# Kernel tuning notes

Measured on AMD Instinct MI355X. Metric: run time of the kernel, lower is better.

Reference implementation:

```python
import jax, jax.numpy as jnp
import numpy as np

B, S, D, H = 4, 2048, 768, 4
DH = D // H  # 192


def setup_inputs() -> dict:
    key = jax.random.key(0)
    ks = jax.random.split(key, 5)
    std = 1.0 / np.sqrt(D)
    return {
        "x": jax.random.normal(ks[0], (B, S, D), dtype=jnp.float32),
        "Wq": jax.random.normal(ks[1], (D, D), dtype=jnp.float32) * std,
        "Wk": jax.random.normal(ks[2], (D, D), dtype=jnp.float32) * std,
        "Wv": jax.random.normal(ks[3], (D, D), dtype=jnp.float32) * std,
        "Wo": jax.random.normal(ks[4], (D, D), dtype=jnp.float32) * std,
    }


def reference(x, Wq, Wk, Wv, Wo):
    b, s, d = x.shape
    # nn.Linear(bias=False): y = x @ W.T
    q = (x @ Wq.T).reshape(b, s, H, DH).transpose(0, 2, 1, 3)  # [B,H,S,DH]
    k = (x @ Wk.T).reshape(b, s, H, DH).transpose(0, 2, 1, 3)
    v = (x @ Wv.T).reshape(b, s, H, DH).transpose(0, 2, 1, 3)
    scale = jnp.sqrt(jnp.asarray(DH, dtype=q.dtype))
    logits = jnp.einsum("bhqd,bhkd->bhqk", q, k) / scale  # [B,H,S,S]
    causal = jnp.tril(jnp.ones((s, s), dtype=bool))
    logits = jnp.where(causal, logits, -jnp.inf)
    A = jax.nn.softmax(logits, axis=-1)
    preout = jnp.einsum("bhqk,bhkd->bhqd", A, v)  # [B,H,S,DH]
    # W_O = rearrange(Wo.T, '(h dh) dm -> h dh dm'); sum over heads == full Wo
    W_O = Wo.T.reshape(H, DH, D)
    out = jnp.einsum("bhsd,hdm->bsm", preout, W_O)  # [B,S,D]
    return out
```

## Files before the change

kernel.cpp:

```cpp
#include <hip/hip_runtime.h>
#include <hip/hip_bf16.h>

constexpr int CB = 4, CS = 2048, CD = 768, CH = 4, CDH = 192;
constexpr int CM = CB * CS;

typedef float f32x4 __attribute__((ext_vector_type(4)));
typedef float fx4 __attribute__((ext_vector_type(4)));
typedef __bf16 bx8 __attribute__((ext_vector_type(8)));
typedef unsigned short u16;
typedef u16 u16x8 __attribute__((ext_vector_type(8)));
typedef u16 u16x4 __attribute__((ext_vector_type(4)));

static __device__ __forceinline__ u16 f32_bf16(float f) {
  unsigned u = __builtin_bit_cast(unsigned, f);
  u += 0x7FFFu + ((u >> 16) & 1u);
  return (u16)(u >> 16);
}
static __device__ __forceinline__ float bf16_f32(u16 v) {
  return __builtin_bit_cast(float, (unsigned)v << 16);
}

static __device__ __forceinline__ f32x4 mfma16(bx8 a, bx8 b, f32x4 c) {
  return __builtin_amdgcn_mfma_f32_16x16x32_bf16(a, b, c, 0, 0, 0);
}

__global__ void __launch_bounds__(256) convert_all(
    const float* __restrict__ x, const float* __restrict__ wq,
    const float* __restrict__ wk, const float* __restrict__ wv,
    const float* __restrict__ wo, u16* __restrict__ xb, u16* __restrict__ wqb,
    u16* __restrict__ wkb, u16* __restrict__ wvb, u16* __restrict__ wob) {
  const float* srcs[5] = {x, wq, wk, wv, wo};
  u16* dsts[5] = {xb, wqb, wkb, wvb, wob};
  const int n4s[5] = {CM * CD / 4, CD * CD / 4, CD * CD / 4, CD * CD / 4,
                      CD * CD / 4};
  const int gsz = gridDim.x * blockDim.x;
  const int gid = blockIdx.x * blockDim.x + threadIdx.x;
#pragma unroll
  for (int sg = 0; sg < 5; ++sg) {
    const fx4* src = (const fx4*)srcs[sg];
    u16* dst = dsts[sg];
    const int n4 = n4s[sg];
    for (int i = gid; i < n4; i += gsz) {
      fx4 v = src[i];
      u16x4 o;
      o[0] = f32_bf16(v[0]);
      o[1] = f32_bf16(v[1]);
      o[2] = f32_bf16(v[2]);
      o[3] = f32_bf16(v[3]);
      *(u16x4*)&dst[(size_t)i * 4] = o;
    }
  }
}

template <bool OUT_BF16>
__global__ void __launch_bounds__(256) gemm_bt(
    const u16* __restrict__ A, const u16* __restrict__ Bw0,
    const u16* __restrict__ Bw1, const u16* __restrict__ Bw2,
    void* __restrict__ C0, void* __restrict__ C1, void* __restrict__ C2,
    int M, int N, int K) {
  constexpr int LDK = 72;
  __shared__ u16 As[128][LDK];
  __shared__ u16 Bs[128][LDK];
  const int z = blockIdx.z;
  const u16* Bw = (z == 0) ? Bw0 : ((z == 1) ? Bw1 : Bw2);
  void* Cv = (z == 0) ? C0 : ((z == 1) ? C1 : C2);
  const int m0 = blockIdx.x * 128;
  const int n0 = blockIdx.y * 128;
  const int tid = threadIdx.x;
  const int wave = tid >> 6, lane = tid & 63;
  const int wr = wave >> 1, wc = wave & 1;
  const int lr = lane & 15, lhi = lane >> 4;

  f32x4 acc[4][4];
  const f32x4 zero = {0.f, 0.f, 0.f, 0.f};
#pragma unroll
  for (int i = 0; i < 4; ++i)
#pragma unroll
    for (int j = 0; j < 4; ++j) acc[i][j] = zero;

  u16x8 areg[4], breg[4];
  auto ldregs = [&](int kk) {
#pragma unroll
    for (int r = 0; r < 4; ++r) {
      const int id = tid + r * 256;
      const int row = id >> 3, ch = id & 7;
      areg[r] = *(const u16x8*)&A[(size_t)(m0 + row) * K + kk + ch * 8];
      breg[r] = *(const u16x8*)&Bw[(size_t)(n0 + row) * K + kk + ch * 8];
    }
  };

  ldregs(0);
  for (int kk = 0; kk < K; kk += 64) {
    __syncthreads();
#pragma unroll
    for (int r = 0; r < 4; ++r) {
      const int id = tid + r * 256;
      const int row = id >> 3, ch = id & 7;
      *(u16x8*)&As[row][ch * 8] = areg[r];
      *(u16x8*)&Bs[row][ch * 8] = breg[r];
    }
    if (kk + 64 < K) ldregs(kk + 64);
    __syncthreads();
#pragma unroll
    for (int ks = 0; ks < 2; ++ks) {
      bx8 af[4], bf[4];
#pragma unroll
      for (int mf = 0; mf < 4; ++mf)
        af[mf] = *(const bx8*)&As[wr * 64 + mf * 16 + lr][ks * 32 + lhi * 8];
#pragma unroll
      for (int nf = 0; nf < 4; ++nf)
        bf[nf] = *(const bx8*)&Bs[wc * 64 + nf * 16 + lr][ks * 32 + lhi * 8];
      __builtin_amdgcn_s_setprio(1);
#pragma unroll
      for (int mf = 0; mf < 4; ++mf)
#pragma unroll
        for (int nf = 0; nf < 4; ++nf)
          acc[mf][nf] = mfma16(af[mf], bf[nf], acc[mf][nf]);
      __builtin_amdgcn_s_setprio(0);
    }
  }
#pragma unroll
  for (int mf = 0; mf < 4; ++mf)
#pragma unroll
    for (int nf = 0; nf < 4; ++nf)
#pragma unroll
      for (int r = 0; r < 4; ++r) {
        const int row = m0 + wr * 64 + mf * 16 + lhi * 4 + r;
        const int col = n0 + wc * 64 + nf * 16 + lr;
        if constexpr (OUT_BF16)
          ((u16*)Cv)[(size_t)row * N + col] = f32_bf16(acc[mf][nf][r]);
        else
          ((float*)Cv)[(size_t)row * N + col] = acc[mf][nf][r];
      }
}

__global__ void __launch_bounds__(256, 2) flash_attn(
    const u16* __restrict__ Qg, const u16* __restrict__ Kg,
    const u16* __restrict__ Vg, u16* __restrict__ Og, u16* __restrict__ paO,
    float* __restrict__ paML, u16* __restrict__ pbO,
    float* __restrict__ pbML) {
  __shared__ u16 Ks[12288];
  __shared__ u16 Vs[12288];
  __shared__ u16 Ps[4][16][72];
  const int i0_ = blockIdx.x;
  const int xcd = i0_ & 7;
  const int j_ = i0_ >> 3;
  const int bh = xcd * 2 + (j_ >> 5);
  const int jj = j_ & 31;
  const int t = jj >> 1;
  const int roleB = jj & 1;
  const int qtLo = t, qtHi = 31 - t;
  const int slot = bh * 16 + (15 - t);
  const int b = bh >> 2, h = bh & 3;
  const int tid = threadIdx.x;
  const int wave = tid >> 6, lane = tid & 63;
  const int lr = lane & 15, lhi = lane >> 4;
  const size_t base_elem = ((size_t)b * CS) * CD + (size_t)h * CDH;
  constexpr float scale = 0.07216878364870323f;
  const f32x4 zero = {0.f, 0.f, 0.f, 0.f};

  int kOff[6], vOff[6];
#pragma unroll
  for (int r = 0; r < 6; ++r) {
    const int p = tid + r * 256;
    {
      const int k = p / 24, c16 = p - k * 24;
      const unsigned swz = ((unsigned)(c16 * 16)) ^ ((unsigned)((k & 7) << 4));
      kOff[r] = k * CD + (int)(swz >> 1);
    }
    {
      const int blk = p >> 3, kq = (p >> 1) & 3, dh = p & 1;
      const int kk = ((blk & 15) << 2) + kq;
      const int d = ((blk >> 4) << 4) + dh * 8;
      vOff[r] = kk * CD + d;
    }
  }
  const unsigned vlds0 =
      (unsigned)(unsigned long long)(__attribute__((address_space(3)))
                                         u16*)&Vs[0];

  float m_run, l_run;
  f32x4 acc[12];
  bx8 qf[6];
  u16x8 kreg[6], vreg[6];

  auto qload = [&](int qt) {
    const size_t qoff = base_elem + (size_t)(qt * 64 + wave * 16 + lr) * CD;
#pragma unroll
    for (int c = 0; c < 6; ++c)
      qf[c] = *(const bx8*)&Qg[qoff + c * 32 + lhi * 8];
  };

  auto ldregs = [&](int kt) {
    const u16* kg = Kg + base_elem + (size_t)(kt * 64) * CD;
    const u16* vg = Vg + base_elem + (size_t)(kt * 64) * CD;
#pragma unroll
    for (int r = 0; r < 6; ++r) {
      kreg[r] = *(const u16x8*)&kg[kOff[r]];
      vreg[r] = *(const u16x8*)&vg[vOff[r]];
    }
  };

  auto compute = [&](int i, int qt) {
    const int qg = qt * 64 + wave * 16 + lr;
    const int k0 = i * 64;
    const bool diag = (i == qt);
    f32x4 st[4];
#pragma unroll
    for (int mf = 0; mf < 4; ++mf) st[mf] = zero;
    __builtin_amdgcn_s_setprio(1);
#pragma unroll
    for (int c = 0; c < 6; ++c)
#pragma unroll
      for (int mf = 0; mf < 4; ++mf) {
        const int row = mf * 16 + lr;
        const unsigned off =
            ((unsigned)(c * 64 + lhi * 16)) ^ ((unsigned)((row & 7) << 4));
        const bx8 kf =
            *(const bx8*)((const char*)Ks + (size_t)row * 384 + off);
        st[mf] = mfma16(kf, qf[c], st[mf]);
      }
    __builtin_amdgcn_s_setprio(0);
    float pvv[16];
#pragma unroll
    for (int mf = 0; mf < 4; ++mf)
#pragma unroll
      for (int r = 0; r < 4; ++r) {
        float s = st[mf][r] * scale;
        if (diag && (k0 + mf * 16 + lhi * 4 + r > qg)) s = -INFINITY;
        pvv[mf * 4 + r] = s;
      }
    float mx = pvv[0];
#pragma unroll
    for (int tt = 1; tt < 16; ++tt) mx = fmaxf(mx, pvv[tt]);
    mx = fmaxf(mx, __shfl_xor(mx, 16, 64));
    mx = fmaxf(mx, __shfl_xor(mx, 32, 64));
    const bool skip = __all(mx - m_run <= 8.0f);
    if (!skip) {
      const float mnew = fmaxf(m_run, mx);
      const float alpha = __expf(m_run - mnew);
      float afr[4];
#pragma unroll
      for (int r = 0; r < 4; ++r) afr[r] = __shfl(alpha, lhi * 4 + r, 64);
#pragma unroll
      for (int nf = 0; nf < 12; ++nf)
#pragma unroll
        for (int r = 0; r < 4; ++r) acc[nf][r] *= afr[r];
      l_run *= alpha;
      m_run = mnew;
    }
    float rs = 0.f;
#pragma unroll
    for (int tt = 0; tt < 16; ++tt) {
      const float e = __expf(pvv[tt] - m_run);
      pvv[tt] = e;
      rs += e;
    }
    rs += __shfl_xor(rs, 16, 64);
    rs += __shfl_xor(rs, 32, 64);
    l_run += rs;
#pragma unroll
    for (int mf = 0; mf < 4; ++mf)
#pragma unroll
      for (int rp = 0; rp < 2; ++rp) {
        const unsigned w0 = f32_bf16(pvv[mf * 4 + rp * 2]);
        const unsigned w1 = f32_bf16(pvv[mf * 4 + rp * 2 + 1]);
        *(unsigned*)&Ps[wave][lr][mf * 16 + lhi * 4 + rp * 2] =
            w0 | (w1 << 16);
      }
    const bx8 pf0 = *(const bx8*)&Ps[wave][lr][lhi * 8];
    const bx8 pf1 = *(const bx8*)&Ps[wave][lr][32 + lhi * 8];
#pragma unroll
    for (int gg = 0; gg < 3; ++gg) {
      u16x4 tl[4][2], th[4][2];
#pragma unroll
      for (int q4 = 0; q4 < 4; ++q4)
#pragma unroll
        for (int c2 = 0; c2 < 2; ++c2) {
          const int nf = gg * 4 + q4;
          const unsigned va =
              vlds0 + (unsigned)((nf * 16 + c2 * 8 + lhi * 2) * 128 + lr * 8);
          asm volatile("ds_read_b64_tr_b16 %0, %2\n\t"
                       "ds_read_b64_tr_b16 %1, %2 offset:128"
                       : "=&v"(tl[q4][c2]), "=&v"(th[q4][c2])
                       : "v"(va));
        }
      asm volatile("s_waitcnt lgkmcnt(0)" ::: "memory");
      __builtin_amdgcn_sched_barrier(0);
      __builtin_amdgcn_s_setprio(1);
#pragma unroll
      for (int q4 = 0; q4 < 4; ++q4)
#pragma unroll
        for (int c2 = 0; c2 < 2; ++c2) {
          const int nf = gg * 4 + q4;
          const u16x8 vv = __builtin_shufflevector(tl[q4][c2], th[q4][c2], 0,
                                                   1, 2, 3, 4, 5, 6, 7);
          acc[nf] = mfma16(c2 == 0 ? pf0 : pf1, __builtin_bit_cast(bx8, vv),
                           acc[nf]);
        }
      __builtin_amdgcn_s_setprio(0);
    }
  };

  auto run = [&](int qt, int i0, int i1) {
    m_run = -INFINITY;
    l_run = 0.f;
#pragma unroll
    for (int nf = 0; nf < 12; ++nf) acc[nf] = zero;
    qload(qt);
    ldregs(i0);
    for (int i = i0; i <= i1; ++i) {
      __syncthreads();
#pragma unroll
      for (int r = 0; r < 6; ++r) {
        *(u16x8*)&Ks[(size_t)(tid + r * 256) * 8] = kreg[r];
        *(u16x8*)&Vs[(size_t)(tid + r * 256) * 8] = vreg[r];
      }
      if (i < i1) ldregs(i + 1);
      __syncthreads();
      compute(i, qt);
    }
  };

  auto final_epilogue = [&](int qt) {
#pragma unroll
    for (int r = 0; r < 4; ++r) {
      const float lb = __shfl(l_run, lhi * 4 + r, 64);
      const float linv = 1.0f / lb;
      const size_t orow =
          base_elem + (size_t)(qt * 64 + wave * 16 + lhi * 4 + r) * CD;
#pragma unroll
      for (int nf = 0; nf < 12; ++nf)
        Og[orow + nf * 16 + lr] = f32_bf16(acc[nf][r] * linv);
    }
  };

  auto partial_epilogue = [&](u16* pO, float* pML) {
    if (lhi == 0) {
      pML[slot * 128 + wave * 16 + lr] = m_run;
      pML[slot * 128 + 64 + wave * 16 + lr] = l_run;
    }
#pragma unroll
    for (int r = 0; r < 4; ++r) {
      const float lb = __shfl(l_run, lhi * 4 + r, 64);
      const float linv = 1.0f / lb;
      u16* dst =
          pO + (size_t)slot * 12288 + (size_t)(wave * 16 + lhi * 4 + r) * 192;
#pragma unroll
      for (int nf = 0; nf < 12; ++nf)
        dst[nf * 16 + lr] = f32_bf16(acc[nf][r] * linv);
    }
  };

  if (roleB) {
    run(qtHi, 15 - t, 31 - t);
    partial_epilogue(pbO, pbML);
  } else {
    run(qtLo, 0, t);
    final_epilogue(qtLo);
    if (t < 15) {
      run(qtHi, 0, 14 - t);
      partial_epilogue(paO, paML);
    } else {
      if (tid < 64) {
        paML[slot * 128 + tid] = -1e30f;
        paML[slot * 128 + 64 + tid] = 0.f;
      }
    }
  }
}

__global__ void __launch_bounds__(256) combine_qt(
    const u16* __restrict__ paO, const float* __restrict__ paML,
    const u16* __restrict__ pbO, const float* __restrict__ pbML,
    u16* __restrict__ Og) {
  const int s = blockIdx.x;
  const int bh = s >> 4;
  const int qtHi = 16 + (s & 15);
  const int b = bh >> 2, h = bh & 3;
  const int tid = threadIdx.x;
  const int row = tid >> 2, cg = tid & 3;
  const float mA = paML[s * 128 + row], lA = paML[s * 128 + 64 + row];
  const float mB = pbML[s * 128 + row], lB = pbML[s * 128 + 64 + row];
  const size_t obase =
      ((size_t)b * CS + (size_t)qtHi * 64 + row) * CD + h * CDH + cg * 48;
  const u16* pa = paO + (size_t)s * 12288 + (size_t)row * 192 + cg * 48;
  const u16* pb = pbO + (size_t)s * 12288 + (size_t)row * 192 + cg * 48;
  if (lA > 0.f) {
    const float M = fmaxf(mA, mB);
    const float wA = lA * __expf(mA - M), wB = lB * __expf(mB - M);
    const float inv = 1.0f / (wA + wB);
    const float fa = wA * inv, fb = wB * inv;
#pragma unroll
    for (int c = 0; c < 6; ++c) {
      const u16x8 va = *(const u16x8*)&pa[c * 8];
      const u16x8 vb = *(const u16x8*)&pb[c * 8];
      u16x8 o;
#pragma unroll
      for (int j = 0; j < 8; ++j)
        o[j] = f32_bf16(fa * bf16_f32(va[j]) + fb * bf16_f32(vb[j]));
      *(u16x8*)&Og[obase + c * 8] = o;
    }
  } else {
#pragma unroll
    for (int c = 0; c < 6; ++c)
      *(u16x8*)&Og[obase + c * 8] = *(const u16x8*)&pb[c * 8];
  }
}

extern "C" void kernel_launch(void* const* d_in, const int* in_sizes, int n_in,
                              void* d_out, int out_size, void* d_ws,
                              size_t ws_size, hipStream_t stream) {
  (void)in_sizes;
  (void)n_in;
  (void)out_size;
  (void)ws_size;
  const float* x = (const float*)d_in[0];
  const float* wq = (const float*)d_in[1];
  const float* wk = (const float*)d_in[2];
  const float* wv = (const float*)d_in[3];
  const float* wo = (const float*)d_in[4];
  float* out = (float*)d_out;
  char* ws = (char*)d_ws;
  const size_t big = (size_t)CM * CD * 2;
  const size_t wsz = (size_t)CD * CD * 2;
  u16* xb = (u16*)ws;
  u16* qb = (u16*)(ws + big);
  u16* kb = (u16*)(ws + 2 * big);
  u16* vb = (u16*)(ws + 3 * big);
  u16* wqb = (u16*)(ws + 4 * big);
  u16* wkb = (u16*)(ws + 4 * big + wsz);
  u16* wvb = (u16*)(ws + 4 * big + 2 * wsz);
  u16* wob = (u16*)(ws + 4 * big + 3 * wsz);
  u16* pob = xb;
  const size_t pOsz = (size_t)256 * 64 * 192 * 2;
  u16* paO = (u16*)d_out;
  u16* pbO = (u16*)((char*)d_out + pOsz);
  float* paML = (float*)((char*)d_out + 2 * pOsz);
  float* pbML = (float*)((char*)d_out + 2 * pOsz + 131072);

  convert_all<<<dim3(1024), dim3(256), 0, stream>>>(x, wq, wk, wv, wo, xb, wqb,
                                                    wkb, wvb, wob);
  gemm_bt<true><<<dim3(64, 6, 3), dim3(256), 0, stream>>>(
      xb, wqb, wkb, wvb, (void*)qb, (void*)kb, (void*)vb, CM, CD, CD);
  flash_attn<<<dim3(512), dim3(256), 0, stream>>>(qb, kb, vb, pob, paO, paML,
                                                  pbO, pbML);
  combine_qt<<<dim3(256), dim3(256), 0, stream>>>(paO, paML, pbO, pbML, pob);
  gemm_bt<false><<<dim3(64, 6, 1), dim3(256), 0, stream>>>(
      pob, wob, wob, wob, (void*)out, (void*)out, (void*)out, CM, CD, CD);
}
```

Measured before the change: 139.2 us.

## Double-buffer K in LDS and split QK/PV phases in flash attention

Adds a second LDS buffer for K so the next K tile is stored while the current one is used. K loads are issued two tiles ahead and V one tile ahead. The compute step is split so the QK^T and softmax phase runs before the barrier and P·V after it, overlapping global loads with compute. P scratch now uses an XOR-swizzled unpadded layout to avoid bank conflicts, and the convert kernel grid is doubled. This raises LDS use per block, which may hurt occupancy at 2 blocks per CU.

```diff
diff --git a/kernel.cpp b/kernel.cpp
--- a/kernel.cpp
+++ b/kernel.cpp
@@ -139,9 +139,9 @@
     const u16* __restrict__ Vg, u16* __restrict__ Og, u16* __restrict__ paO,
     float* __restrict__ paML, u16* __restrict__ pbO,
     float* __restrict__ pbML) {
-  __shared__ u16 Ks[12288];
+  __shared__ u16 Kbuf[2][12288];
   __shared__ u16 Vs[12288];
-  __shared__ u16 Ps[4][16][72];
+  __shared__ u16 Ps[4][16][64];
   const int i0_ = blockIdx.x;
   const int xcd = i0_ & 7;
   const int j_ = i0_ >> 3;
@@ -191,20 +191,22 @@
       qf[c] = *(const bx8*)&Qg[qoff + c * 32 + lhi * 8];
   };
 
-  auto ldregs = [&](int kt) {
+  auto kload = [&](int kt) {
     const u16* kg = Kg + base_elem + (size_t)(kt * 64) * CD;
+#pragma unroll
+    for (int r = 0; r < 6; ++r) kreg[r] = *(const u16x8*)&kg[kOff[r]];
+  };
+  auto vload = [&](int kt) {
     const u16* vg = Vg + base_elem + (size_t)(kt * 64) * CD;
 #pragma unroll
-    for (int r = 0; r < 6; ++r) {
-      kreg[r] = *(const u16x8*)&kg[kOff[r]];
-      vreg[r] = *(const u16x8*)&vg[vOff[r]];
-    }
-  };
-
-  auto compute = [&](int i, int qt) {
+    for (int r = 0; r < 6; ++r) vreg[r] = *(const u16x8*)&vg[vOff[r]];
+  };
+
+  auto compute_qkt_sm = [&](int i, int qt, int cur) {
     const int qg = qt * 64 + wave * 16 + lr;
     const int k0 = i * 64;
     const bool diag = (i == qt);
+    const char* ksb = (const char*)&Kbuf[cur][0];
     f32x4 st[4];
 #pragma unroll
     for (int mf = 0; mf < 4; ++mf) st[mf] = zero;
@@ -216,8 +218,7 @@
         const int row = mf * 16 + lr;
         const unsigned off =
             ((unsigned)(c * 64 + lhi * 16)) ^ ((unsigned)((row & 7) << 4));
-        const bx8 kf =
-            *(const bx8*)((const char*)Ks + (size_t)row * 384 + off);
+        const bx8 kf = *(const bx8*)(ksb + (size_t)row * 384 + off);
         st[mf] = mfma16(kf, qf[c], st[mf]);
       }
     __builtin_amdgcn_s_setprio(0);
@@ -265,11 +266,18 @@
       for (int rp = 0; rp < 2; ++rp) {
         const unsigned w0 = f32_bf16(pvv[mf * 4 + rp * 2]);
         const unsigned w1 = f32_bf16(pvv[mf * 4 + rp * 2 + 1]);
-        *(unsigned*)&Ps[wave][lr][mf * 16 + lhi * 4 + rp * 2] =
-            w0 | (w1 << 16);
-      }
-    const bx8 pf0 = *(const bx8*)&Ps[wave][lr][lhi * 8];
-    const bx8 pf1 = *(const bx8*)&Ps[wave][lr][32 + lhi * 8];
+        const unsigned pbyte =
+            (unsigned)(wave * 2048 + lr * 128 +
+                       ((mf * 32 + lhi * 8 + rp * 4) ^ ((lr & 7) << 4)));
+        *(unsigned*)((char*)Ps + pbyte) = w0 | (w1 << 16);
+      }
+  };
+
+  auto compute_pv = [&]() {
+    const bx8 pf0 = *(const bx8*)((const char*)Ps + wave * 2048 + lr * 128 +
+                                  ((lhi * 16) ^ ((lr & 7) << 4)));
+    const bx8 pf1 = *(const bx8*)((const char*)Ps + wave * 2048 + lr * 128 +
+                                  ((64 + lhi * 16) ^ ((lr & 7) << 4)));
 #pragma unroll
     for (int gg = 0; gg < 3; ++gg) {
       u16x4 tl[4][2], th[4][2];
@@ -308,17 +316,30 @@
 #pragma unroll
     for (int nf = 0; nf < 12; ++nf) acc[nf] = zero;
     qload(qt);
-    ldregs(i0);
+    kload(i0);
+    __syncthreads();
+#pragma unroll
+    for (int r = 0; r < 6; ++r)
+      *(u16x8*)&Kbuf[0][(size_t)(tid + r * 256) * 8] = kreg[r];
+    vload(i0);
+    if (i0 + 1 <= i1) kload(i0 + 1);
+    int cur = 0;
     for (int i = i0; i <= i1; ++i) {
       __syncthreads();
 #pragma unroll
-      for (int r = 0; r < 6; ++r) {
-        *(u16x8*)&Ks[(size_t)(tid + r * 256) * 8] = kreg[r];
+      for (int r = 0; r < 6; ++r)
         *(u16x8*)&Vs[(size_t)(tid + r * 256) * 8] = vreg[r];
-      }
-      if (i < i1) ldregs(i + 1);
+      if (i < i1) {
+#pragma unroll
+        for (int r = 0; r < 6; ++r)
+          *(u16x8*)&Kbuf[cur ^ 1][(size_t)(tid + r * 256) * 8] = kreg[r];
+        vload(i + 1);
+      }
+      if (i + 2 <= i1) kload(i + 2);
+      compute_qkt_sm(i, qt, cur);
       __syncthreads();
-      compute(i, qt);
+      compute_pv();
+      cur ^= 1;
     }
   };
 
@@ -439,7 +460,7 @@
   float* paML = (float*)((char*)d_out + 2 * pOsz);
   float* pbML = (float*)((char*)d_out + 2 * pOsz + 131072);
 
-  convert_all<<<dim3(1024), dim3(256), 0, stream>>>(x, wq, wk, wv, wo, xb, wqb,
+  convert_all<<<dim3(2048), dim3(256), 0, stream>>>(x, wq, wk, wv, wo, xb, wqb,
                                                     wkb, wvb, wob);
   gemm_bt<true><<<dim3(64, 6, 3), dim3(256), 0, stream>>>(
       xb, wqb, wkb, wvb, (void*)qb, (void*)kb, (void*)vb, CM, CD, CD);
```

New measurement: 156.4 us. +12.4%, slower.

## Double-buffer GEMM tiles with direct global-to-LDS loads and XOR swizzle

Applied to the files above, without the earlier changes.

The bf16 GEMM now stages A/B tiles straight from global memory into LDS using global_load_lds, instead of going through registers. It double-buffers the tiles so the next K-slice loads while MFMAs run on the current one. It also XOR-swizzles the LDS layout in place of row padding, to avoid bank conflicts. The convert kernel grid is doubled. LDS use rises to 64KB per block, which may lower occupancy, and the single barrier per iteration relies on the hardware waiting for the direct LDS loads to finish.

```diff
diff --git a/kernel.cpp b/kernel.cpp
--- a/kernel.cpp
+++ b/kernel.cpp
@@ -22,6 +22,12 @@
 
 static __device__ __forceinline__ f32x4 mfma16(bx8 a, bx8 b, f32x4 c) {
   return __builtin_amdgcn_mfma_f32_16x16x32_bf16(a, b, c, 0, 0, 0);
+}
+
+static __device__ __forceinline__ void load_lds16(const u16* g, u16* l) {
+  __builtin_amdgcn_global_load_lds(
+      (const __attribute__((address_space(1))) unsigned int*)g,
+      (__attribute__((address_space(3))) unsigned int*)l, 16, 0, 0);
 }
 
 __global__ void __launch_bounds__(256) convert_all(
@@ -58,9 +64,8 @@
     const u16* __restrict__ Bw1, const u16* __restrict__ Bw2,
     void* __restrict__ C0, void* __restrict__ C1, void* __restrict__ C2,
     int M, int N, int K) {
-  constexpr int LDK = 72;
-  __shared__ u16 As[128][LDK];
-  __shared__ u16 Bs[128][LDK];
+  __shared__ u16 As[2][8192];
+  __shared__ u16 Bs[2][8192];
   const int z = blockIdx.z;
   const u16* Bw = (z == 0) ? Bw0 : ((z == 1) ? Bw1 : Bw2);
   void* Cv = (z == 0) ? C0 : ((z == 1) ? C1 : C2);
@@ -78,38 +83,47 @@
 #pragma unroll
     for (int j = 0; j < 4; ++j) acc[i][j] = zero;
 
-  u16x8 areg[4], breg[4];
-  auto ldregs = [&](int kk) {
+  int sOff[4];
+#pragma unroll
+  for (int r = 0; r < 4; ++r) {
+    const int p = tid + r * 256;
+    const int row = p >> 3, ch = p & 7;
+    sOff[r] = row * K +
+              (int)(((unsigned)(ch * 16) ^ ((unsigned)((row & 7) << 4))) >> 1);
+  }
+  const u16* Ag = A + (size_t)m0 * K;
+  const u16* Bg = Bw + (size_t)n0 * K;
+
+  auto stage = [&](int buf, int kk) {
 #pragma unroll
     for (int r = 0; r < 4; ++r) {
-      const int id = tid + r * 256;
-      const int row = id >> 3, ch = id & 7;
-      areg[r] = *(const u16x8*)&A[(size_t)(m0 + row) * K + kk + ch * 8];
-      breg[r] = *(const u16x8*)&Bw[(size_t)(n0 + row) * K + kk + ch * 8];
-    }
-  };
-
-  ldregs(0);
+      load_lds16(Ag + kk + sOff[r], &As[buf][(size_t)(tid + r * 256) * 8]);
+      load_lds16(Bg + kk + sOff[r], &Bs[buf][(size_t)(tid + r * 256) * 8]);
+    }
+  };
+
+  stage(0, 0);
+  __syncthreads();
+  int buf = 0;
   for (int kk = 0; kk < K; kk += 64) {
-    __syncthreads();
-#pragma unroll
-    for (int r = 0; r < 4; ++r) {
-      const int id = tid + r * 256;
-      const int row = id >> 3, ch = id & 7;
-      *(u16x8*)&As[row][ch * 8] = areg[r];
-      *(u16x8*)&Bs[row][ch * 8] = breg[r];
-    }
-    if (kk + 64 < K) ldregs(kk + 64);
-    __syncthreads();
+    if (kk + 64 < K) stage(buf ^ 1, kk + 64);
 #pragma unroll
     for (int ks = 0; ks < 2; ++ks) {
       bx8 af[4], bf[4];
 #pragma unroll
-      for (int mf = 0; mf < 4; ++mf)
-        af[mf] = *(const bx8*)&As[wr * 64 + mf * 16 + lr][ks * 32 + lhi * 8];
-#pragma unroll
-      for (int nf = 0; nf < 4; ++nf)
-        bf[nf] = *(const bx8*)&Bs[wc * 64 + nf * 16 + lr][ks * 32 + lhi * 8];
+      for (int mf = 0; mf < 4; ++mf) {
+        const int row = wr * 64 + mf * 16 + lr;
+        const unsigned off =
+            ((unsigned)(ks * 64 + lhi * 16)) ^ ((unsigned)((row & 7) << 4));
+        af[mf] = *(const bx8*)((const char*)&As[buf][0] + row * 128 + off);
+      }
+#pragma unroll
+      for (int nf = 0; nf < 4; ++nf) {
+        const int row = wc * 64 + nf * 16 + lr;
+        const unsigned off =
+            ((unsigned)(ks * 64 + lhi * 16)) ^ ((unsigned)((row & 7) << 4));
+        bf[nf] = *(const bx8*)((const char*)&Bs[buf][0] + row * 128 + off);
+      }
       __builtin_amdgcn_s_setprio(1);
 #pragma unroll
       for (int mf = 0; mf < 4; ++mf)
@@ -118,6 +132,8 @@
           acc[mf][nf] = mfma16(af[mf], bf[nf], acc[mf][nf]);
       __builtin_amdgcn_s_setprio(0);
     }
+    __syncthreads();
+    buf ^= 1;
   }
 #pragma unroll
   for (int mf = 0; mf < 4; ++mf)
@@ -439,7 +455,7 @@
   float* paML = (float*)((char*)d_out + 2 * pOsz);
   float* pbML = (float*)((char*)d_out + 2 * pOsz + 131072);
 
-  convert_all<<<dim3(1024), dim3(256), 0, stream>>>(x, wq, wk, wv, wo, xb, wqb,
+  convert_all<<<dim3(2048), dim3(256), 0, stream>>>(x, wq, wk, wv, wo, xb, wqb,
                                                     wkb, wvb, wob);
   gemm_bt<true><<<dim3(64, 6, 3), dim3(256), 0, stream>>>(
       xb, wqb, wkb, wvb, (void*)qb, (void*)kb, (void*)vb, CM, CD, CD);
```

Measured after the change: 145.3 us. 4.4% more time.
